# Performance work log

Measured on AMD Instinct MI355X. Metric: run time of the kernel, lower is better.

## Reference

```python
import jax, jax.numpy as jnp
import numpy as np


def setup_inputs() -> dict:
    key = jax.random.key(0)
    k1, k2 = jax.random.split(key)
    B, C, Q, D = 32, 4096, 512, 512
    similarity_matrix = jax.random.normal(k1, (B, C, Q), dtype=jnp.float32)
    encoded_question = jax.random.normal(k2, (B, Q, D), dtype=jnp.float32)
    return {"similarity_matrix": similarity_matrix, "encoded_question": encoded_question}


def reference(similarity_matrix, encoded_question):
    # softmax over query axis, then attention-weighted sum of question encodings.
    # Equivalent to the original expand_dims/multiply/sum, but fused as a matmul.
    attn = jax.nn.softmax(similarity_matrix, axis=-1)          # [B, C, Q]
    out = jnp.einsum('bcq,bqd->bcd', attn, encoded_question)   # [B, C, D]
    return out
```

## Files before the change

### kernel.cpp

```cpp
#include <hip/hip_runtime.h>
#include <hip/hip_bf16.h>


constexpr int Bn = 32;
constexpr int Cn = 4096;
constexpr int Qn = 512;
constexpr int Dn = 512;

typedef __attribute__((ext_vector_type(8))) short short8;
typedef __attribute__((ext_vector_type(4))) float floatx4;

__device__ __forceinline__ ushort f2bf(float f) {
  union { float f; unsigned u; } v; v.f = f;
  unsigned r = v.u + 0x7FFFu + ((v.u >> 16) & 1u);
  return (ushort)(r >> 16);
}

__device__ __forceinline__ uint4 exp_pack(float4 x, float4 y, float& rsum) {
  float e0 = __expf(x.x), e1 = __expf(x.y), e2 = __expf(x.z), e3 = __expf(x.w);
  float e4 = __expf(y.x), e5 = __expf(y.y), e6 = __expf(y.z), e7 = __expf(y.w);
  rsum += ((e0 + e1) + (e2 + e3)) + ((e4 + e5) + (e6 + e7));
  uint4 pk;
  pk.x = (uint)f2bf(e0) | ((uint)f2bf(e1) << 16);
  pk.y = (uint)f2bf(e2) | ((uint)f2bf(e3) << 16);
  pk.z = (uint)f2bf(e4) | ((uint)f2bf(e5) << 16);
  pk.w = (uint)f2bf(e6) | ((uint)f2bf(e7) << 16);
  return pk;
}

__global__ __launch_bounds__(256) void enc_to_frag(const float* __restrict__ E,
                                                   ushort* __restrict__ Etf) {
  const int ks = blockIdx.x, b = blockIdx.y;
  const int t = threadIdx.x;
  const int lane = t & 63, grp = t >> 6;
  const int l16 = lane & 15, lhi = lane >> 4;
  const float* src = E + ((size_t)b * Qn + ks * 32 + lhi * 8) * Dn + l16;
#pragma unroll
  for (int dt8 = 0; dt8 < 8; ++dt8) {
    int dt = grp * 8 + dt8;
    float e[8];
#pragma unroll
    for (int j = 0; j < 8; ++j) e[j] = src[(size_t)j * Dn + dt * 16];
    uint4 pk;
    pk.x = (uint)f2bf(e[0]) | ((uint)f2bf(e[1]) << 16);
    pk.y = (uint)f2bf(e[2]) | ((uint)f2bf(e[3]) << 16);
    pk.z = (uint)f2bf(e[4]) | ((uint)f2bf(e[5]) << 16);
    pk.w = (uint)f2bf(e[6]) | ((uint)f2bf(e[7]) << 16);
    *(uint4*)((char*)Etf + (((size_t)(b * 32 + dt) * 16 + ks) * 64 + lane) * 16) = pk;
  }
}

__global__ __launch_bounds__(512, 2) void c2q_fused(const float* __restrict__ sim,
                                                    const ushort* __restrict__ Etf,
                                                    float* __restrict__ out) {
  __shared__ char Abuf[2][64 * 128];
  __shared__ float rsInv[64];

  const int tid  = threadIdx.x;
  const int lane = tid & 63;
  const int wid  = tid >> 6;
  const int l16  = lane & 15;
  const int lhi  = lane >> 4;

  const int lin = blockIdx.x;
  const int blo = lin & 7;
  const int bhi = (lin >> 3) & 3;
  const int mt  = lin >> 5;
  const int b   = bhi * 8 + blo;
  const int c0  = mt * 64;

  const int srow = tid >> 3;
  const int so   = tid & 7;
  const float* sload = sim + ((size_t)b * Cn + c0 + srow) * Qn + so * 8;
  const int swa = (srow * 128 + so * 16) ^ ((srow & 7) << 4);

  const short8* EB = (const short8*)Etf + ((size_t)(b * 32 + wid * 4) * 16) * 64 + lane;

  float rsum = 0.0f;
  floatx4 acc[4][4] = {};
  float4 vs[2][2];
  short8 bfr[2][4];

  vs[0][0] = *(const float4*)(sload);
  vs[0][1] = *(const float4*)(sload + 4);
  vs[1][0] = *(const float4*)(sload + 64);
  vs[1][1] = *(const float4*)(sload + 68);
#pragma unroll
  for (int nr = 0; nr < 4; ++nr) {
    bfr[0][nr] = EB[((size_t)nr * 16 + 0) * 64];
    bfr[1][nr] = EB[((size_t)nr * 16 + 1) * 64];
  }
  *(uint4*)(Abuf[0] + swa) = exp_pack(vs[0][0], vs[0][1], rsum);
  __syncthreads();

#pragma unroll
  for (int t = 0; t < 8; ++t) {
    if (t < 6) {
      vs[t & 1][0] = *(const float4*)(sload + (t + 2) * 64);
      vs[t & 1][1] = *(const float4*)(sload + (t + 2) * 64 + 4);
    }
    __builtin_amdgcn_sched_barrier(0);

#pragma unroll
    for (int ks = 0; ks < 2; ++ks) {
      const int kidx = 2 * t + ks;
      short8 a[4];
#pragma unroll
      for (int mr = 0; mr < 4; ++mr) {
        int row = mr * 16 + l16;
        a[mr] = *(const short8*)(Abuf[t & 1] +
                 ((row * 128 + ks * 64 + lhi * 16) ^ ((row & 7) << 4)));
      }
      __builtin_amdgcn_s_setprio(1);
#pragma unroll
      for (int mr = 0; mr < 4; ++mr)
#pragma unroll
        for (int nr = 0; nr < 4; ++nr)
          acc[mr][nr] = __builtin_amdgcn_mfma_f32_16x16x32_bf16(
              a[mr], bfr[kidx & 1][nr], acc[mr][nr], 0, 0, 0);
      __builtin_amdgcn_s_setprio(0);
      if (kidx < 14) {
#pragma unroll
        for (int nr = 0; nr < 4; ++nr)
          bfr[kidx & 1][nr] = EB[((size_t)nr * 16 + kidx + 2) * 64];
      }
    }

    if (t < 7) {
      *(uint4*)(Abuf[(t + 1) & 1] + swa) =
          exp_pack(vs[(t + 1) & 1][0], vs[(t + 1) & 1][1], rsum);
    } else {
      rsum += __shfl_xor(rsum, 1);
      rsum += __shfl_xor(rsum, 2);
      rsum += __shfl_xor(rsum, 4);
      if (so == 0) rsInv[srow] = 1.0f / rsum;
    }
    __syncthreads();
  }

  float* outp = out + ((size_t)b * Cn + c0) * Dn + wid * 64;
#pragma unroll
  for (int mr = 0; mr < 4; ++mr) {
    float rs[4];
#pragma unroll
    for (int rr = 0; rr < 4; ++rr) rs[rr] = rsInv[mr * 16 + lhi * 4 + rr];
#pragma unroll
    for (int nr = 0; nr < 4; ++nr) {
#pragma unroll
      for (int rr = 0; rr < 4; ++rr) {
        int row = mr * 16 + lhi * 4 + rr;
        outp[(size_t)row * Dn + nr * 16 + l16] = acc[mr][nr][rr] * rs[rr];
      }
    }
  }
}

extern "C" void kernel_launch(void* const* d_in, const int* in_sizes, int n_in,
                              void* d_out, int out_size, void* d_ws, size_t ws_size,
                              hipStream_t stream) {
  const float* sim = (const float*)d_in[0];
  const float* enc = (const float*)d_in[1];
  float* outp = (float*)d_out;
  ushort* Etf = (ushort*)d_ws;

  enc_to_frag<<<dim3(16, Bn), 256, 0, stream>>>(enc, Etf);
  c2q_fused<<<dim3(2048), 512, 0, stream>>>(sim, Etf, outp);
}
```

Baseline: 165.6 us.

## Make fused softmax-matmul kernel loop over eight row tiles per block

The grid shrinks from 2048 blocks to 256, and each block now walks eight consecutive 64-row tiles of the same batch. The next tile's first similarity loads and encoder fragments are issued before the current tile's output stores, so reading the next tile overlaps writing the current one. `__syncthreads` is replaced by a barrier that waits only on LDS counters, not outstanding global loads. The risk is fewer resident blocks per CU, hence less latency hiding and possible load imbalance.

```diff
diff --git a/kernel.cpp b/kernel.cpp
--- a/kernel.cpp
+++ b/kernel.cpp
@@ -27,6 +27,14 @@
   pk.w = (uint)f2bf(e6) | ((uint)f2bf(e7) << 16);
   return pk;
 }
+
+#define BARRIER_NODRAIN() do {                                   \
+  __builtin_amdgcn_sched_barrier(0);                             \
+  asm volatile("s_waitcnt lgkmcnt(0)" ::: "memory");             \
+  __builtin_amdgcn_s_barrier();                                  \
+  asm volatile("" ::: "memory");                                 \
+  __builtin_amdgcn_sched_barrier(0);                             \
+} while (0)
 
 __global__ __launch_bounds__(256) void enc_to_frag(const float* __restrict__ E,
                                                    ushort* __restrict__ Etf) {
@@ -65,19 +73,17 @@
   const int lin = blockIdx.x;
   const int blo = lin & 7;
   const int bhi = (lin >> 3) & 3;
-  const int mt  = lin >> 5;
+  const int g   = lin >> 5;
   const int b   = bhi * 8 + blo;
-  const int c0  = mt * 64;
 
   const int srow = tid >> 3;
   const int so   = tid & 7;
-  const float* sload = sim + ((size_t)b * Cn + c0 + srow) * Qn + so * 8;
+  const float* sload = sim + ((size_t)b * Cn + g * 512 + srow) * Qn + so * 8;
+  float*       outp  = out + ((size_t)b * Cn + g * 512) * Dn + wid * 64;
   const int swa = (srow * 128 + so * 16) ^ ((srow & 7) << 4);
 
   const short8* EB = (const short8*)Etf + ((size_t)(b * 32 + wid * 4) * 16) * 64 + lane;
 
-  float rsum = 0.0f;
-  floatx4 acc[4][4] = {};
   float4 vs[2][2];
   short8 bfr[2][4];
 
@@ -87,71 +93,94 @@
   vs[1][1] = *(const float4*)(sload + 68);
 #pragma unroll
   for (int nr = 0; nr < 4; ++nr) {
-    bfr[0][nr] = EB[((size_t)nr * 16 + 0) * 64];
+    bfr[0][nr] = EB[((size_t)nr * 16) * 64];
     bfr[1][nr] = EB[((size_t)nr * 16 + 1) * 64];
   }
-  *(uint4*)(Abuf[0] + swa) = exp_pack(vs[0][0], vs[0][1], rsum);
-  __syncthreads();
+
+#pragma unroll 1
+  for (int p = 0; p < 8; ++p) {
+    float rsum = 0.0f;
+    floatx4 acc[4][4] = {};
+
+    *(uint4*)(Abuf[0] + swa) = exp_pack(vs[0][0], vs[0][1], rsum);
+    BARRIER_NODRAIN();
 
 #pragma unroll
-  for (int t = 0; t < 8; ++t) {
-    if (t < 6) {
-      vs[t & 1][0] = *(const float4*)(sload + (t + 2) * 64);
-      vs[t & 1][1] = *(const float4*)(sload + (t + 2) * 64 + 4);
+    for (int t = 0; t < 8; ++t) {
+      if (t < 6) {
+        vs[t & 1][0] = *(const float4*)(sload + (t + 2) * 64);
+        vs[t & 1][1] = *(const float4*)(sload + (t + 2) * 64 + 4);
+      }
+      __builtin_amdgcn_sched_barrier(0);
+
+#pragma unroll
+      for (int ks = 0; ks < 2; ++ks) {
+        const int kidx = 2 * t + ks;
+        short8 a[4];
+#pragma unroll
+        for (int mr = 0; mr < 4; ++mr) {
+          int row = mr * 16 + l16;
+          a[mr] = *(const short8*)(Abuf[t & 1] +
+                   ((row * 128 + ks * 64 + lhi * 16) ^ ((row & 7) << 4)));
+        }
+        __builtin_amdgcn_s_setprio(1);
+#pragma unroll
+        for (int mr = 0; mr < 4; ++mr)
+#pragma unroll
+          for (int nr = 0; nr < 4; ++nr)
+            acc[mr][nr] = __builtin_amdgcn_mfma_f32_16x16x32_bf16(
+                a[mr], bfr[kidx & 1][nr], acc[mr][nr], 0, 0, 0);
+        __builtin_amdgcn_s_setprio(0);
+        if (kidx < 14) {
+#pragma unroll
+          for (int nr = 0; nr < 4; ++nr)
+            bfr[kidx & 1][nr] = EB[((size_t)nr * 16 + kidx + 2) * 64];
+        }
+      }
+
+      if (t < 7) {
+        *(uint4*)(Abuf[(t + 1) & 1] + swa) =
+            exp_pack(vs[(t + 1) & 1][0], vs[(t + 1) & 1][1], rsum);
+      } else {
+        rsum += __shfl_xor(rsum, 1);
+        rsum += __shfl_xor(rsum, 2);
+        rsum += __shfl_xor(rsum, 4);
+        if (so == 0) rsInv[srow] = 1.0f / rsum;
+      }
+      BARRIER_NODRAIN();
+    }
+
+    if (p < 7) {
+      const float* nsl = sload + (size_t)64 * Qn;
+      vs[0][0] = *(const float4*)(nsl);
+      vs[0][1] = *(const float4*)(nsl + 4);
+      vs[1][0] = *(const float4*)(nsl + 64);
+      vs[1][1] = *(const float4*)(nsl + 68);
+#pragma unroll
+      for (int nr = 0; nr < 4; ++nr) {
+        bfr[0][nr] = EB[((size_t)nr * 16) * 64];
+        bfr[1][nr] = EB[((size_t)nr * 16 + 1) * 64];
+      }
     }
     __builtin_amdgcn_sched_barrier(0);
 
 #pragma unroll
-    for (int ks = 0; ks < 2; ++ks) {
-      const int kidx = 2 * t + ks;
-      short8 a[4];
+    for (int mr = 0; mr < 4; ++mr) {
+      float rs[4];
 #pragma unroll
-      for (int mr = 0; mr < 4; ++mr) {
-        int row = mr * 16 + l16;
-        a[mr] = *(const short8*)(Abuf[t & 1] +
-                 ((row * 128 + ks * 64 + lhi * 16) ^ ((row & 7) << 4)));
-      }
-      __builtin_amdgcn_s_setprio(1);
+      for (int rr = 0; rr < 4; ++rr) rs[rr] = rsInv[mr * 16 + lhi * 4 + rr];
 #pragma unroll
-      for (int mr = 0; mr < 4; ++mr)
+      for (int nr = 0; nr < 4; ++nr) {
 #pragma unroll
-        for (int nr = 0; nr < 4; ++nr)
-          acc[mr][nr] = __builtin_amdgcn_mfma_f32_16x16x32_bf16(
-              a[mr], bfr[kidx & 1][nr], acc[mr][nr], 0, 0, 0);
-      __builtin_amdgcn_s_setprio(0);
-      if (kidx < 14) {
-#pragma unroll
-        for (int nr = 0; nr < 4; ++nr)
-          bfr[kidx & 1][nr] = EB[((size_t)nr * 16 + kidx + 2) * 64];
+        for (int rr = 0; rr < 4; ++rr) {
+          int row = mr * 16 + lhi * 4 + rr;
+          outp[(size_t)row * Dn + nr * 16 + l16] = acc[mr][nr][rr] * rs[rr];
+        }
       }
     }
 
-    if (t < 7) {
-      *(uint4*)(Abuf[(t + 1) & 1] + swa) =
-          exp_pack(vs[(t + 1) & 1][0], vs[(t + 1) & 1][1], rsum);
-    } else {
-      rsum += __shfl_xor(rsum, 1);
-      rsum += __shfl_xor(rsum, 2);
-      rsum += __shfl_xor(rsum, 4);
-      if (so == 0) rsInv[srow] = 1.0f / rsum;
-    }
-    __syncthreads();
-  }
-
-  float* outp = out + ((size_t)b * Cn + c0) * Dn + wid * 64;
-#pragma unroll
-  for (int mr = 0; mr < 4; ++mr) {
-    float rs[4];
-#pragma unroll
-    for (int rr = 0; rr < 4; ++rr) rs[rr] = rsInv[mr * 16 + lhi * 4 + rr];
-#pragma unroll
-    for (int nr = 0; nr < 4; ++nr) {
-#pragma unroll
-      for (int rr = 0; rr < 4; ++rr) {
-        int row = mr * 16 + lhi * 4 + rr;
-        outp[(size_t)row * Dn + nr * 16 + l16] = acc[mr][nr][rr] * rs[rr];
-      }
-    }
+    sload += (size_t)64 * Qn;
+    outp  += (size_t)64 * Dn;
   }
 }
 
@@ -164,5 +193,5 @@
   ushort* Etf = (ushort*)d_ws;
 
   enc_to_frag<<<dim3(16, Bn), 256, 0, stream>>>(enc, Etf);
-  c2q_fused<<<dim3(2048), 512, 0, stream>>>(sim, Etf, outp);
+  c2q_fused<<<dim3(256), 512, 0, stream>>>(sim, Etf, outp);
 }
```

Measured after the change: 380.9 us. 2.3x slower.
